# Optimization experiments

Measured on AMD Instinct MI355X. Metric: run time of the kernel, lower is better.

The kernel has to match this reference:

```python
import jax, jax.numpy as jnp
import numpy as np

NUM_EMBEDDINGS = 1024
EMBEDDING_DIM = 64
COMMITMENT_COST = 0.25
N_TOKENS = 131072


def setup_inputs() -> dict:
    key = jax.random.key(0)
    k_in, k_emb = jax.random.split(key)
    inputs = jax.random.normal(k_in, (N_TOKENS, EMBEDDING_DIM), dtype=jnp.float32)
    # torch init: uniform(-1/K, 1/K)
    codebook = jax.random.uniform(
        k_emb, (NUM_EMBEDDINGS, EMBEDDING_DIM), dtype=jnp.float32,
        minval=-1.0 / NUM_EMBEDDINGS, maxval=1.0 / NUM_EMBEDDINGS)
    return {"inputs": inputs, "codebook": codebook}


def reference(inputs, codebook):
    sg = jax.lax.stop_gradient
    distances = (jnp.sum(inputs * inputs, axis=1, keepdims=True)
                 - 2.0 * jnp.matmul(inputs, codebook.T)
                 + jnp.sum(codebook * codebook, axis=1)[None, :])
    encoding_indices = jnp.argmin(distances, axis=1)          # [N]
    # direct gather (same math as one-hot @ codebook)
    quantized = jnp.take(codebook, encoding_indices, axis=0)  # [N, D]
    # original computes e_latent_loss and q_latent_loss identically
    # (both mse(inputs, quantized.detach())), so loss = (1 + beta) * mse
    mse = jnp.mean((sg(quantized) - inputs) ** 2)
    loss = mse + COMMITMENT_COST * mse
    # straight-through estimator
    quantized_st = inputs + sg(quantized - inputs)
    # perplexity from code usage histogram (== mean of one-hot encodings)
    counts = jax.ops.segment_sum(
        jnp.ones((inputs.shape[0],), dtype=jnp.float32),
        encoding_indices, num_segments=NUM_EMBEDDINGS)
    avg_probs = counts / inputs.shape[0]
    perplexity = jnp.exp(-jnp.sum(avg_probs * jnp.log(avg_probs + 1e-10)))
    return loss, quantized_st, perplexity, encoding_indices[:, None]
```

## Files before the change

kernel.cpp:

```cpp
#include <hip/hip_runtime.h>
#include <math.h>

#define NTOK 131072
#define KC   1024
#define DIMV 64
#define NWAVE 8
#define TPW  64
#define TPB  512
#define CMAX 256
#define EPSH 1e-3f

#define OUT_LOSS 0
#define OUT_Q    1
#define OUT_PERP (1 + NTOK * DIMV)
#define OUT_IDX  (2 + NTOK * DIMV)

typedef __attribute__((ext_vector_type(8))) short short8;
typedef __attribute__((ext_vector_type(4))) float f32x4;

__device__ __forceinline__ float sumsq64_np(const float v[DIMV]) {
#pragma clang fp contract(off)
  {
    float r[8];
#pragma unroll
    for (int j = 0; j < 8; ++j) r[j] = v[j] * v[j];
#pragma unroll
    for (int i = 8; i < 64; i += 8) {
#pragma unroll
      for (int j = 0; j < 8; ++j) r[j] += v[i + j] * v[i + j];
    }
    return ((r[0] + r[1]) + (r[2] + r[3])) + ((r[4] + r[5]) + (r[6] + r[7]));
  }
}

__device__ __forceinline__ unsigned short bf16rne(float f) {
  unsigned int u = __float_as_uint(f);
  return (unsigned short)((u + 0x7fffu + ((u >> 16) & 1u)) >> 16);
}

__global__ void __launch_bounds__(512)
vq_fused(const float* __restrict__ xin, const float* __restrict__ cb,
         float* __restrict__ out, float* __restrict__ ws) {
  __shared__ __align__(16) char s_pack[131072];
  __shared__ float s_norm[KC];
  __shared__ unsigned int s_hist[KC];
  __shared__ unsigned int s_cand[NWAVE][CMAX];
  __shared__ unsigned long long s_key[NWAVE][TPW];
  __shared__ int s_cnt[NWAVE];
  __shared__ int s_last;

  const int tid = threadIdx.x;
  const int l   = tid & 63;
  const int wv  = tid >> 6;
  const int cls = l & 15;
  const int g   = l >> 4;
  const int blk = blockIdx.x;
  const int tb  = blk * TPB + wv * TPW;

  float* ws_mse = ws;
  unsigned int* ws_hist = (unsigned int*)ws + 1;
  unsigned int* ws_done = (unsigned int*)ws + 1 + KC;

  for (int c = tid; c < 8192; c += 512) {
    const int tile = c >> 7, f = (c >> 6) & 1, cl = c & 63;
    const int code = tile * 16 + (cl & 15);
    const int kb = f * 32 + (cl >> 4) * 8;
    const float4* src = (const float4*)(cb + code * DIMV + kb);
    float4 v0 = src[0], v1 = src[1];
    float v[8] = {v0.x, v0.y, v0.z, v0.w, v1.x, v1.y, v1.z, v1.w};
    unsigned int hw[4];
#pragma unroll
    for (int j = 0; j < 4; ++j) {
      hw[j] = (unsigned int)bf16rne(v[2 * j]) |
              ((unsigned int)bf16rne(v[2 * j + 1]) << 16);
    }
    *(uint4*)(s_pack + tile * 2048 + f * 1024 + cl * 16) =
        make_uint4(hw[0], hw[1], hw[2], hw[3]);
  }
  for (int k = tid; k < KC; k += 512) {
    float row[DIMV];
    const float4* r4 = (const float4*)(cb + (size_t)k * DIMV);
#pragma unroll
    for (int i = 0; i < 16; ++i) {
      float4 t = r4[i];
      row[4 * i + 0] = t.x; row[4 * i + 1] = t.y;
      row[4 * i + 2] = t.z; row[4 * i + 3] = t.w;
    }
    s_norm[k] = sumsq64_np(row);
    s_hist[k] = 0u;
  }
  s_key[wv][l] = ~0ull;
  if (tid < NWAVE) s_cnt[tid] = 0;

  short8 af[4][2];
#pragma unroll
  for (int grp = 0; grp < 4; ++grp) {
    const float* xr = xin + (size_t)(tb + grp * 16 + cls) * DIMV + g * 8;
#pragma unroll
    for (int kc = 0; kc < 2; ++kc) {
      float4 v0 = *(const float4*)(xr + kc * 32);
      float4 v1 = *(const float4*)(xr + kc * 32 + 4);
      float vv[8] = {v0.x, v0.y, v0.z, v0.w, v1.x, v1.y, v1.z, v1.w};
#pragma unroll
      for (int j = 0; j < 8; ++j) af[grp][kc][j] = (short)bf16rne(vv[j]);
    }
  }
  __syncthreads();

  float minv[4][4];
#pragma unroll
  for (int grp = 0; grp < 4; ++grp)
#pragma unroll
    for (int j = 0; j < 4; ++j) minv[grp][j] = INFINITY;

  short8 b0 = *(const short8*)(s_pack + l * 16);
  short8 b1 = *(const short8*)(s_pack + 1024 + l * 16);
  float nr = s_norm[cls];
#pragma unroll 2
  for (int t = 0; t < 63; ++t) {
    short8 c0 = b0, c1 = b1;
    float cc = -0.5f * nr;
    const char* bp = s_pack + (t + 1) * 2048 + l * 16;
    b0 = *(const short8*)(bp);
    b1 = *(const short8*)(bp + 1024);
    nr = s_norm[(t + 1) * 16 + cls];
#pragma unroll
    for (int grp = 0; grp < 4; ++grp) {
      f32x4 acc = {cc, cc, cc, cc};
      acc = __builtin_amdgcn_mfma_f32_16x16x32_bf16(af[grp][0], c0, acc, 0, 0, 0);
      acc = __builtin_amdgcn_mfma_f32_16x16x32_bf16(af[grp][1], c1, acc, 0, 0, 0);
#pragma unroll
      for (int j = 0; j < 4; ++j)
        minv[grp][j] = fminf(minv[grp][j], -acc[j]);
    }
  }
  {
    float cc = -0.5f * nr;
#pragma unroll
    for (int grp = 0; grp < 4; ++grp) {
      f32x4 acc = {cc, cc, cc, cc};
      acc = __builtin_amdgcn_mfma_f32_16x16x32_bf16(af[grp][0], b0, acc, 0, 0, 0);
      acc = __builtin_amdgcn_mfma_f32_16x16x32_bf16(af[grp][1], b1, acc, 0, 0, 0);
#pragma unroll
      for (int j = 0; j < 4; ++j)
        minv[grp][j] = fminf(minv[grp][j], -acc[j]);
    }
  }
#pragma unroll
  for (int mask = 1; mask < 16; mask <<= 1) {
#pragma unroll
    for (int grp = 0; grp < 4; ++grp)
#pragma unroll
      for (int j = 0; j < 4; ++j)
        minv[grp][j] = fminf(minv[grp][j], __shfl_xor(minv[grp][j], mask, 64));
  }
  float thr[4][4];
#pragma unroll
  for (int grp = 0; grp < 4; ++grp)
#pragma unroll
    for (int j = 0; j < 4; ++j) thr[grp][j] = minv[grp][j] + EPSH;

  b0 = *(const short8*)(s_pack + l * 16);
  b1 = *(const short8*)(s_pack + 1024 + l * 16);
  nr = s_norm[cls];
#pragma unroll 2
  for (int t = 0; t < 64; ++t) {
    short8 c0 = b0, c1 = b1;
    float cc = -0.5f * nr;
    if (t < 63) {
      const char* bp = s_pack + (t + 1) * 2048 + l * 16;
      b0 = *(const short8*)(bp);
      b1 = *(const short8*)(bp + 1024);
      nr = s_norm[(t + 1) * 16 + cls];
    }
#pragma unroll
    for (int grp = 0; grp < 4; ++grp) {
      f32x4 acc = {cc, cc, cc, cc};
      acc = __builtin_amdgcn_mfma_f32_16x16x32_bf16(af[grp][0], c0, acc, 0, 0, 0);
      acc = __builtin_amdgcn_mfma_f32_16x16x32_bf16(af[grp][1], c1, acc, 0, 0, 0);
#pragma unroll
      for (int j = 0; j < 4; ++j) {
        if (-acc[j] <= thr[grp][j]) {
          int pos = atomicAdd(&s_cnt[wv], 1);
          if (pos < CMAX)
            s_cand[wv][pos] =
                ((unsigned int)(grp * 16 + g * 4 + j) << 10) |
                (unsigned int)(t * 16 + cls);
        }
      }
    }
  }
  asm volatile("s_waitcnt lgkmcnt(0)" ::: "memory");
  const int cnt = s_cnt[wv];
  int n = cnt < CMAX ? cnt : CMAX;

  for (int base = 0; base < n; base += 64) {
    int i = base + l;
    if (i < n) {
      unsigned int pk = s_cand[wv][i];
      int m = (int)(pk >> 10), k = (int)(pk & 1023);
      const float4* xr4 = (const float4*)(xin + (size_t)(tb + m) * DIMV);
      const float4* er4 = (const float4*)(cb + (size_t)k * DIMV);
      float r[8];
      float dot = 0.0f;
#pragma unroll
      for (int s = 0; s < 8; ++s) {
        float4 a = xr4[2 * s], b = xr4[2 * s + 1];
        float4 ea = er4[2 * s], eb = er4[2 * s + 1];
        float xv[8] = {a.x, a.y, a.z, a.w, b.x, b.y, b.z, b.w};
        float ev[8] = {ea.x, ea.y, ea.z, ea.w, eb.x, eb.y, eb.z, eb.w};
        {
#pragma clang fp contract(off)
#pragma unroll
          for (int j = 0; j < 8; ++j) {
            float sq = xv[j] * xv[j];
            r[j] = (s == 0) ? sq : (r[j] + sq);
          }
        }
#pragma unroll
        for (int j = 0; j < 8; ++j) dot = __builtin_fmaf(ev[j], xv[j], dot);
      }
      float xx = ((r[0] + r[1]) + (r[2] + r[3])) + ((r[4] + r[5]) + (r[6] + r[7]));
      float d = (xx - 2.0f * dot) + s_norm[k];
      unsigned long long key =
          ((unsigned long long)__float_as_uint(d) << 10) | (unsigned long long)k;
      atomicMin(&s_key[wv][m], key);
    }
  }

  if (cnt > CMAX) {
    asm volatile("s_waitcnt lgkmcnt(0)" ::: "memory");
    const int m = l;
    float xv[DIMV];
    const float4* xr4 = (const float4*)(xin + (size_t)(tb + m) * DIMV);
#pragma unroll
    for (int i = 0; i < 16; ++i) {
      float4 t4 = xr4[i];
      xv[4 * i + 0] = t4.x; xv[4 * i + 1] = t4.y;
      xv[4 * i + 2] = t4.z; xv[4 * i + 3] = t4.w;
    }
    float xx = sumsq64_np(xv);
    float bd = INFINITY; int bk = 0;
    for (int k = 0; k < KC; ++k) {
      const float* e = cb + (size_t)k * DIMV;
      float dot = 0.0f;
#pragma unroll
      for (int i = 0; i < DIMV; ++i) dot = __builtin_fmaf(e[i], xv[i], dot);
      float d = (xx - 2.0f * dot) + s_norm[k];
      if (d < bd) { bd = d; bk = k; }
    }
    s_key[wv][m] =
        ((unsigned long long)__float_as_uint(bd) << 10) | (unsigned long long)bk;
  }
  asm volatile("s_waitcnt lgkmcnt(0)" ::: "memory");

  {
    const int token = tb + l;
    unsigned long long key = s_key[wv][l];
    const int bk = (int)(key & 1023ull);
    out[OUT_IDX + token] = (float)bk;
    atomicAdd(&s_hist[bk], 1u);
    const float4* q4 = (const float4*)(cb + (size_t)bk * DIMV);
    const float4* x4 = (const float4*)(xin + (size_t)token * DIMV);
    float* oq = out + OUT_Q + (size_t)token * DIMV;
    float mse_part = 0.0f;
#pragma unroll
    for (int rr = 0; rr < 16; ++rr) {
      float4 qv = q4[rr], xv = x4[rr];
      float d0 = qv.x - xv.x, d1 = qv.y - xv.y;
      float d2 = qv.z - xv.z, d3 = qv.w - xv.w;
      float4 o;
      o.x = xv.x + d0; o.y = xv.y + d1; o.z = xv.z + d2; o.w = xv.w + d3;
      mse_part = __builtin_fmaf(d0, d0, mse_part);
      mse_part = __builtin_fmaf(d1, d1, mse_part);
      mse_part = __builtin_fmaf(d2, d2, mse_part);
      mse_part = __builtin_fmaf(d3, d3, mse_part);
      *(float4*)(oq + 4 * rr) = o;
    }
#pragma unroll
    for (int mask = 1; mask < 64; mask <<= 1)
      mse_part += __shfl_xor(mse_part, mask, 64);
    if (l == 0) atomicAdd(ws_mse, mse_part);
  }

  __syncthreads();
  for (int k = tid; k < KC; k += 512) {
    unsigned int c = s_hist[k];
    if (c) atomicAdd(&ws_hist[k], c);
  }
  __syncthreads();

  if (tid == 0) {
    __threadfence();
    unsigned int tkt = atomicAdd(ws_done, 1u);
    s_last = (tkt == (unsigned int)(gridDim.x - 1)) ? 1 : 0;
  }
  __syncthreads();
  if (s_last) {
    __threadfence();
    float term = 0.0f;
    for (int k = tid; k < KC; k += 512) {
      unsigned int c = atomicAdd(&ws_hist[k], 0u);
      float p = (float)c / 131072.0f;
      term += p * logf(p + 1e-10f);
    }
    s_norm[tid] = term;
    __syncthreads();
#pragma unroll
    for (int s = 256; s > 0; s >>= 1) {
      if (tid < s) s_norm[tid] += s_norm[tid + s];
      __syncthreads();
    }
    if (tid == 0) {
      out[OUT_PERP] = expf(-s_norm[0]);
      float mse = atomicAdd(ws_mse, 0.0f) / 8388608.0f;
      out[OUT_LOSS] = mse + 0.25f * mse;
    }
  }
}

extern "C" void kernel_launch(void* const* d_in, const int* in_sizes, int n_in,
                              void* d_out, int out_size, void* d_ws, size_t ws_size,
                              hipStream_t stream) {
  (void)in_sizes; (void)n_in; (void)out_size; (void)ws_size;
  const float* xin = (const float*)d_in[0];
  const float* cb  = (const float*)d_in[1];
  float* out = (float*)d_out;
  float* ws  = (float*)d_ws;

  hipMemsetAsync(d_ws, 0, sizeof(float) * (1 + KC + 1), stream);
  hipLaunchKernelGGL(vq_fused, dim3(NTOK / TPB), dim3(512), 0, stream,
                     xin, cb, out, ws);
}
```

Baseline: 203.7 us.

## Split codebook scan across wave pairs with 1024-thread blocks

Doubles the block to 1024 threads so that each group of 64 tokens is handled by two waves, each scanning half of the codebook tiles. Per-wave minima are merged through shared memory before the candidate-threshold pass. The epilogue then has two threads per token writing halves of the output row. This aims to raise the number of waves per CU and cut per-wave MFMA latency, given that the 131 KB codebook in shared memory limits the CU to one block. The cost is extra block-wide syncs, a smaller candidate buffer per wave that makes the slow fallback path more likely, and higher register pressure under the 1024-thread launch bound.

```diff
diff --git a/kernel.cpp b/kernel.cpp
--- a/kernel.cpp
+++ b/kernel.cpp
@@ -4,10 +4,8 @@
 #define NTOK 131072
 #define KC   1024
 #define DIMV 64
-#define NWAVE 8
-#define TPW  64
 #define TPB  512
-#define CMAX 256
+#define CMAX 128
 #define EPSH 1e-3f
 
 #define OUT_LOSS 0
@@ -38,15 +36,17 @@
   return (unsigned short)((u + 0x7fffu + ((u >> 16) & 1u)) >> 16);
 }
 
-__global__ void __launch_bounds__(512)
+__global__ void __launch_bounds__(1024)
 vq_fused(const float* __restrict__ xin, const float* __restrict__ cb,
          float* __restrict__ out, float* __restrict__ ws) {
   __shared__ __align__(16) char s_pack[131072];
   __shared__ float s_norm[KC];
   __shared__ unsigned int s_hist[KC];
-  __shared__ unsigned int s_cand[NWAVE][CMAX];
-  __shared__ unsigned long long s_key[NWAVE][TPW];
-  __shared__ int s_cnt[NWAVE];
+  __shared__ float s_pmin[16][64];
+  __shared__ float s_gmin[8][64];
+  __shared__ unsigned int s_cand[16][CMAX];
+  __shared__ unsigned long long s_key[8][64];
+  __shared__ int s_cnt[16];
   __shared__ int s_last;
 
   const int tid = threadIdx.x;
@@ -54,14 +54,16 @@
   const int wv  = tid >> 6;
   const int cls = l & 15;
   const int g   = l >> 4;
+  const int q   = wv >> 1;
+  const int wl  = wv & 1;
   const int blk = blockIdx.x;
-  const int tb  = blk * TPB + wv * TPW;
+  const int tb  = blk * TPB + q * 64;
 
   float* ws_mse = ws;
   unsigned int* ws_hist = (unsigned int*)ws + 1;
   unsigned int* ws_done = (unsigned int*)ws + 1 + KC;
 
-  for (int c = tid; c < 8192; c += 512) {
+  for (int c = tid; c < 8192; c += 1024) {
     const int tile = c >> 7, f = (c >> 6) & 1, cl = c & 63;
     const int code = tile * 16 + (cl & 15);
     const int kb = f * 32 + (cl >> 4) * 8;
@@ -77,7 +79,8 @@
     *(uint4*)(s_pack + tile * 2048 + f * 1024 + cl * 16) =
         make_uint4(hw[0], hw[1], hw[2], hw[3]);
   }
-  for (int k = tid; k < KC; k += 512) {
+  {
+    const int k = tid;
     float row[DIMV];
     const float4* r4 = (const float4*)(cb + (size_t)k * DIMV);
 #pragma unroll
@@ -89,8 +92,8 @@
     s_norm[k] = sumsq64_np(row);
     s_hist[k] = 0u;
   }
-  s_key[wv][l] = ~0ull;
-  if (tid < NWAVE) s_cnt[tid] = 0;
+  if (tid < 512) s_key[tid >> 6][tid & 63] = ~0ull;
+  if (tid < 16) s_cnt[tid] = 0;
 
   short8 af[4][2];
 #pragma unroll
@@ -107,23 +110,26 @@
   }
   __syncthreads();
 
+  const int tbase = wl * 32;
   float minv[4][4];
 #pragma unroll
   for (int grp = 0; grp < 4; ++grp)
 #pragma unroll
     for (int j = 0; j < 4; ++j) minv[grp][j] = INFINITY;
 
-  short8 b0 = *(const short8*)(s_pack + l * 16);
-  short8 b1 = *(const short8*)(s_pack + 1024 + l * 16);
-  float nr = s_norm[cls];
+  short8 b0 = *(const short8*)(s_pack + tbase * 2048 + l * 16);
+  short8 b1 = *(const short8*)(s_pack + tbase * 2048 + 1024 + l * 16);
+  float nr = s_norm[tbase * 16 + cls];
 #pragma unroll 2
-  for (int t = 0; t < 63; ++t) {
+  for (int t = 0; t < 32; ++t) {
     short8 c0 = b0, c1 = b1;
     float cc = -0.5f * nr;
-    const char* bp = s_pack + (t + 1) * 2048 + l * 16;
-    b0 = *(const short8*)(bp);
-    b1 = *(const short8*)(bp + 1024);
-    nr = s_norm[(t + 1) * 16 + cls];
+    if (t < 31) {
+      const char* bp = s_pack + (tbase + t + 1) * 2048 + l * 16;
+      b0 = *(const short8*)(bp);
+      b1 = *(const short8*)(bp + 1024);
+      nr = s_norm[(tbase + t + 1) * 16 + cls];
+    }
 #pragma unroll
     for (int grp = 0; grp < 4; ++grp) {
       f32x4 acc = {cc, cc, cc, cc};
@@ -134,18 +140,6 @@
         minv[grp][j] = fminf(minv[grp][j], -acc[j]);
     }
   }
-  {
-    float cc = -0.5f * nr;
-#pragma unroll
-    for (int grp = 0; grp < 4; ++grp) {
-      f32x4 acc = {cc, cc, cc, cc};
-      acc = __builtin_amdgcn_mfma_f32_16x16x32_bf16(af[grp][0], b0, acc, 0, 0, 0);
-      acc = __builtin_amdgcn_mfma_f32_16x16x32_bf16(af[grp][1], b1, acc, 0, 0, 0);
-#pragma unroll
-      for (int j = 0; j < 4; ++j)
-        minv[grp][j] = fminf(minv[grp][j], -acc[j]);
-    }
-  }
 #pragma unroll
   for (int mask = 1; mask < 16; mask <<= 1) {
 #pragma unroll
@@ -154,24 +148,38 @@
       for (int j = 0; j < 4; ++j)
         minv[grp][j] = fminf(minv[grp][j], __shfl_xor(minv[grp][j], mask, 64));
   }
-  float thr[4][4];
-#pragma unroll
-  for (int grp = 0; grp < 4; ++grp)
-#pragma unroll
-    for (int j = 0; j < 4; ++j) thr[grp][j] = minv[grp][j] + EPSH;
-
-  b0 = *(const short8*)(s_pack + l * 16);
-  b1 = *(const short8*)(s_pack + 1024 + l * 16);
-  nr = s_norm[cls];
+  if (cls == 0) {
+#pragma unroll
+    for (int grp = 0; grp < 4; ++grp) {
+      float4 v = make_float4(minv[grp][0], minv[grp][1], minv[grp][2], minv[grp][3]);
+      *(float4*)&s_pmin[wv][grp * 16 + g * 4] = v;
+    }
+  }
+  __syncthreads();
+  if (tid < 512) {
+    const int q2 = tid >> 6, m = tid & 63;
+    s_gmin[q2][m] = fminf(s_pmin[q2 * 2][m], s_pmin[q2 * 2 + 1][m]);
+  }
+  __syncthreads();
+#pragma unroll
+  for (int grp = 0; grp < 4; ++grp) {
+    float4 t4 = *(const float4*)&s_gmin[q][grp * 16 + g * 4];
+    minv[grp][0] = t4.x + EPSH; minv[grp][1] = t4.y + EPSH;
+    minv[grp][2] = t4.z + EPSH; minv[grp][3] = t4.w + EPSH;
+  }
+
+  b0 = *(const short8*)(s_pack + tbase * 2048 + l * 16);
+  b1 = *(const short8*)(s_pack + tbase * 2048 + 1024 + l * 16);
+  nr = s_norm[tbase * 16 + cls];
 #pragma unroll 2
-  for (int t = 0; t < 64; ++t) {
+  for (int t = 0; t < 32; ++t) {
     short8 c0 = b0, c1 = b1;
     float cc = -0.5f * nr;
-    if (t < 63) {
-      const char* bp = s_pack + (t + 1) * 2048 + l * 16;
+    if (t < 31) {
+      const char* bp = s_pack + (tbase + t + 1) * 2048 + l * 16;
       b0 = *(const short8*)(bp);
       b1 = *(const short8*)(bp + 1024);
-      nr = s_norm[(t + 1) * 16 + cls];
+      nr = s_norm[(tbase + t + 1) * 16 + cls];
     }
 #pragma unroll
     for (int grp = 0; grp < 4; ++grp) {
@@ -180,12 +188,12 @@
       acc = __builtin_amdgcn_mfma_f32_16x16x32_bf16(af[grp][1], c1, acc, 0, 0, 0);
 #pragma unroll
       for (int j = 0; j < 4; ++j) {
-        if (-acc[j] <= thr[grp][j]) {
+        if (-acc[j] <= minv[grp][j]) {
           int pos = atomicAdd(&s_cnt[wv], 1);
           if (pos < CMAX)
             s_cand[wv][pos] =
                 ((unsigned int)(grp * 16 + g * 4 + j) << 10) |
-                (unsigned int)(t * 16 + cls);
+                (unsigned int)((tbase + t) * 16 + cls);
         }
       }
     }
@@ -224,12 +232,11 @@
       float d = (xx - 2.0f * dot) + s_norm[k];
       unsigned long long key =
           ((unsigned long long)__float_as_uint(d) << 10) | (unsigned long long)k;
-      atomicMin(&s_key[wv][m], key);
+      atomicMin(&s_key[q][m], key);
     }
   }
 
   if (cnt > CMAX) {
-    asm volatile("s_waitcnt lgkmcnt(0)" ::: "memory");
     const int m = l;
     float xv[DIMV];
     const float4* xr4 = (const float4*)(xin + (size_t)(tb + m) * DIMV);
@@ -241,7 +248,7 @@
     }
     float xx = sumsq64_np(xv);
     float bd = INFINITY; int bk = 0;
-    for (int k = 0; k < KC; ++k) {
+    for (int k = wl * 512; k < wl * 512 + 512; ++k) {
       const float* e = cb + (size_t)k * DIMV;
       float dot = 0.0f;
 #pragma unroll
@@ -249,23 +256,27 @@
       float d = (xx - 2.0f * dot) + s_norm[k];
       if (d < bd) { bd = d; bk = k; }
     }
-    s_key[wv][m] =
+    unsigned long long key =
         ((unsigned long long)__float_as_uint(bd) << 10) | (unsigned long long)bk;
-  }
-  asm volatile("s_waitcnt lgkmcnt(0)" ::: "memory");
+    atomicMin(&s_key[q][m], key);
+  }
+  __syncthreads();
 
   {
-    const int token = tb + l;
-    unsigned long long key = s_key[wv][l];
+    const int tok = tid >> 1, h = tid & 1;
+    const int token = blk * TPB + tok;
+    unsigned long long key = s_key[tok >> 6][tok & 63];
     const int bk = (int)(key & 1023ull);
-    out[OUT_IDX + token] = (float)bk;
-    atomicAdd(&s_hist[bk], 1u);
-    const float4* q4 = (const float4*)(cb + (size_t)bk * DIMV);
-    const float4* x4 = (const float4*)(xin + (size_t)token * DIMV);
-    float* oq = out + OUT_Q + (size_t)token * DIMV;
+    if (h == 0) {
+      out[OUT_IDX + token] = (float)bk;
+      atomicAdd(&s_hist[bk], 1u);
+    }
+    const float4* q4 = (const float4*)(cb + (size_t)bk * DIMV + h * 32);
+    const float4* x4 = (const float4*)(xin + (size_t)token * DIMV + h * 32);
+    float* oq = out + OUT_Q + (size_t)token * DIMV + h * 32;
     float mse_part = 0.0f;
 #pragma unroll
-    for (int rr = 0; rr < 16; ++rr) {
+    for (int rr = 0; rr < 8; ++rr) {
       float4 qv = q4[rr], xv = x4[rr];
       float d0 = qv.x - xv.x, d1 = qv.y - xv.y;
       float d2 = qv.z - xv.z, d3 = qv.w - xv.w;
@@ -282,13 +293,11 @@
       mse_part += __shfl_xor(mse_part, mask, 64);
     if (l == 0) atomicAdd(ws_mse, mse_part);
   }
-
-  __syncthreads();
-  for (int k = tid; k < KC; k += 512) {
-    unsigned int c = s_hist[k];
-    if (c) atomicAdd(&ws_hist[k], c);
-  }
-  __syncthreads();
+  __syncthreads();
+  {
+    unsigned int c = s_hist[tid];
+    if (c) atomicAdd(&ws_hist[tid], c);
+  }
 
   if (tid == 0) {
     __threadfence();
@@ -298,16 +307,12 @@
   __syncthreads();
   if (s_last) {
     __threadfence();
-    float term = 0.0f;
-    for (int k = tid; k < KC; k += 512) {
-      unsigned int c = atomicAdd(&ws_hist[k], 0u);
-      float p = (float)c / 131072.0f;
-      term += p * logf(p + 1e-10f);
-    }
-    s_norm[tid] = term;
+    unsigned int c = atomicAdd(&ws_hist[tid], 0u);
+    float p = (float)c / 131072.0f;
+    s_norm[tid] = p * logf(p + 1e-10f);
     __syncthreads();
 #pragma unroll
-    for (int s = 256; s > 0; s >>= 1) {
+    for (int s = 512; s > 0; s >>= 1) {
       if (tid < s) s_norm[tid] += s_norm[tid + s];
       __syncthreads();
     }
@@ -329,6 +334,6 @@
   float* ws  = (float*)d_ws;
 
   hipMemsetAsync(d_ws, 0, sizeof(float) * (1 + KC + 1), stream);
-  hipLaunchKernelGGL(vq_fused, dim3(NTOK / TPB), dim3(512), 0, stream,
+  hipLaunchKernelGGL(vq_fused, dim3(NTOK / TPB), dim3(1024), 0, stream,
                      xin, cb, out, ws);
 }
```

New measurement: 216.4 us. 6.2% more time.

## Precompute bf16 codebook pack in separate kernel and use 1024-thread blocks

Applied to the files above, without the earlier changes.

Moves the per-block bf16 codebook packing and norm computation into a small pre-kernel that writes to workspace, so each main block only copies the packed codebook into LDS. The main kernel switches to 16 waves of 32 tokens (1024 threads per block), which spreads the packing cost over more tokens and gives more waves per CU for the MFMA loops. It also replaces the memset with zeroing done in the pre-kernel. The trade-off is an extra launch, fewer independent MFMA groups per wave, and a smaller candidate buffer that may hit the slow fallback more often.

```diff
diff --git a/kernel.cpp b/kernel.cpp
--- a/kernel.cpp
+++ b/kernel.cpp
@@ -4,10 +4,10 @@
 #define NTOK 131072
 #define KC   1024
 #define DIMV 64
-#define NWAVE 8
-#define TPW  64
-#define TPB  512
-#define CMAX 256
+#define NWAVE 16
+#define TPW  32
+#define TPB  (NWAVE * TPW)
+#define CMAX 128
 #define EPSH 1e-3f
 
 #define OUT_LOSS 0
@@ -15,6 +15,11 @@
 #define OUT_PERP (1 + NTOK * DIMV)
 #define OUT_IDX  (2 + NTOK * DIMV)
 
+#define WS_HIST 1
+#define WS_TKT  1025
+#define WS_NORM 1026
+#define WS_PACK_BYTES 12288
+
 typedef __attribute__((ext_vector_type(8))) short short8;
 typedef __attribute__((ext_vector_type(4))) float f32x4;
 
@@ -38,9 +43,41 @@
   return (unsigned short)((u + 0x7fffu + ((u >> 16) & 1u)) >> 16);
 }
 
-__global__ void __launch_bounds__(512)
-vq_fused(const float* __restrict__ xin, const float* __restrict__ cb,
-         float* __restrict__ out, float* __restrict__ ws) {
+__global__ void __launch_bounds__(256)
+vq_pack_kernel(const float* __restrict__ cb, float* __restrict__ ws) {
+  const int e = blockIdx.x * 256 + threadIdx.x;
+  if (e < 1026) ws[e] = 0.0f;
+  const int tile = e >> 7, f = (e >> 6) & 1, l = e & 63;
+  const int code = tile * 16 + (l & 15);
+  const int kb = f * 32 + (l >> 4) * 8;
+  const float4* src = reinterpret_cast<const float4*>(cb + code * DIMV + kb);
+  float4 v0 = src[0], v1 = src[1];
+  float v[8] = {v0.x, v0.y, v0.z, v0.w, v1.x, v1.y, v1.z, v1.w};
+  unsigned int hw[4];
+#pragma unroll
+  for (int j = 0; j < 4; ++j) {
+    hw[j] = (unsigned int)bf16rne(v[2 * j]) |
+            ((unsigned int)bf16rne(v[2 * j + 1]) << 16);
+  }
+  char* pack = (char*)ws + WS_PACK_BYTES;
+  *(uint4*)(pack + tile * 2048 + f * 1024 + l * 16) =
+      make_uint4(hw[0], hw[1], hw[2], hw[3]);
+  if (e < KC) {
+    float row[DIMV];
+    const float4* r4 = reinterpret_cast<const float4*>(cb + e * DIMV);
+#pragma unroll
+    for (int i = 0; i < 16; ++i) {
+      float4 t = r4[i];
+      row[4 * i + 0] = t.x; row[4 * i + 1] = t.y;
+      row[4 * i + 2] = t.z; row[4 * i + 3] = t.w;
+    }
+    ws[WS_NORM + e] = sumsq64_np(row);
+  }
+}
+
+__global__ void __launch_bounds__(1024)
+vq_main_mfma(const float* __restrict__ xin, const float* __restrict__ cb,
+             float* __restrict__ out, float* __restrict__ ws) {
   __shared__ __align__(16) char s_pack[131072];
   __shared__ float s_norm[KC];
   __shared__ unsigned int s_hist[KC];
@@ -58,43 +95,26 @@
   const int tb  = blk * TPB + wv * TPW;
 
   float* ws_mse = ws;
-  unsigned int* ws_hist = (unsigned int*)ws + 1;
-  unsigned int* ws_done = (unsigned int*)ws + 1 + KC;
-
-  for (int c = tid; c < 8192; c += 512) {
-    const int tile = c >> 7, f = (c >> 6) & 1, cl = c & 63;
-    const int code = tile * 16 + (cl & 15);
-    const int kb = f * 32 + (cl >> 4) * 8;
-    const float4* src = (const float4*)(cb + code * DIMV + kb);
-    float4 v0 = src[0], v1 = src[1];
-    float v[8] = {v0.x, v0.y, v0.z, v0.w, v1.x, v1.y, v1.z, v1.w};
-    unsigned int hw[4];
-#pragma unroll
-    for (int j = 0; j < 4; ++j) {
-      hw[j] = (unsigned int)bf16rne(v[2 * j]) |
-              ((unsigned int)bf16rne(v[2 * j + 1]) << 16);
-    }
-    *(uint4*)(s_pack + tile * 2048 + f * 1024 + cl * 16) =
-        make_uint4(hw[0], hw[1], hw[2], hw[3]);
-  }
-  for (int k = tid; k < KC; k += 512) {
-    float row[DIMV];
-    const float4* r4 = (const float4*)(cb + (size_t)k * DIMV);
-#pragma unroll
-    for (int i = 0; i < 16; ++i) {
-      float4 t = r4[i];
-      row[4 * i + 0] = t.x; row[4 * i + 1] = t.y;
-      row[4 * i + 2] = t.z; row[4 * i + 3] = t.w;
-    }
-    s_norm[k] = sumsq64_np(row);
-    s_hist[k] = 0u;
-  }
-  s_key[wv][l] = ~0ull;
+  unsigned int* ws_hist = (unsigned int*)ws + WS_HIST;
+  unsigned int* ws_done = (unsigned int*)ws + WS_TKT;
+  const float* ws_norm = ws + WS_NORM;
+  const char* pack = (const char*)ws + WS_PACK_BYTES;
+
+  {
+    const uint4* src = (const uint4*)pack;
+    uint4* dst = (uint4*)s_pack;
+#pragma unroll
+    for (int i = 0; i < 8; ++i) dst[tid + i * 1024] = src[tid + i * 1024];
+  }
+  s_norm[tid] = ws_norm[tid];
+  s_hist[tid] = 0u;
+  if (tid < NWAVE * TPW) s_key[tid >> 5][tid & 31] = ~0ull;
   if (tid < NWAVE) s_cnt[tid] = 0;
-
-  short8 af[4][2];
-#pragma unroll
-  for (int grp = 0; grp < 4; ++grp) {
+  __syncthreads();
+
+  short8 af[2][2];
+#pragma unroll
+  for (int grp = 0; grp < 2; ++grp) {
     const float* xr = xin + (size_t)(tb + grp * 16 + cls) * DIMV + g * 8;
 #pragma unroll
     for (int kc = 0; kc < 2; ++kc) {
@@ -105,11 +125,10 @@
       for (int j = 0; j < 8; ++j) af[grp][kc][j] = (short)bf16rne(vv[j]);
     }
   }
-  __syncthreads();
-
-  float minv[4][4];
-#pragma unroll
-  for (int grp = 0; grp < 4; ++grp)
+
+  float minv[2][4];
+#pragma unroll
+  for (int grp = 0; grp < 2; ++grp)
 #pragma unroll
     for (int j = 0; j < 4; ++j) minv[grp][j] = INFINITY;
 
@@ -117,15 +136,17 @@
   short8 b1 = *(const short8*)(s_pack + 1024 + l * 16);
   float nr = s_norm[cls];
 #pragma unroll 2
-  for (int t = 0; t < 63; ++t) {
+  for (int t = 0; t < 64; ++t) {
     short8 c0 = b0, c1 = b1;
     float cc = -0.5f * nr;
-    const char* bp = s_pack + (t + 1) * 2048 + l * 16;
-    b0 = *(const short8*)(bp);
-    b1 = *(const short8*)(bp + 1024);
-    nr = s_norm[(t + 1) * 16 + cls];
-#pragma unroll
-    for (int grp = 0; grp < 4; ++grp) {
+    if (t < 63) {
+      const char* bp = s_pack + (t + 1) * 2048 + l * 16;
+      b0 = *(const short8*)(bp);
+      b1 = *(const short8*)(bp + 1024);
+      nr = s_norm[(t + 1) * 16 + cls];
+    }
+#pragma unroll
+    for (int grp = 0; grp < 2; ++grp) {
       f32x4 acc = {cc, cc, cc, cc};
       acc = __builtin_amdgcn_mfma_f32_16x16x32_bf16(af[grp][0], c0, acc, 0, 0, 0);
       acc = __builtin_amdgcn_mfma_f32_16x16x32_bf16(af[grp][1], c1, acc, 0, 0, 0);
@@ -134,29 +155,17 @@
         minv[grp][j] = fminf(minv[grp][j], -acc[j]);
     }
   }
-  {
-    float cc = -0.5f * nr;
-#pragma unroll
-    for (int grp = 0; grp < 4; ++grp) {
-      f32x4 acc = {cc, cc, cc, cc};
-      acc = __builtin_amdgcn_mfma_f32_16x16x32_bf16(af[grp][0], b0, acc, 0, 0, 0);
-      acc = __builtin_amdgcn_mfma_f32_16x16x32_bf16(af[grp][1], b1, acc, 0, 0, 0);
-#pragma unroll
-      for (int j = 0; j < 4; ++j)
-        minv[grp][j] = fminf(minv[grp][j], -acc[j]);
-    }
-  }
 #pragma unroll
   for (int mask = 1; mask < 16; mask <<= 1) {
 #pragma unroll
-    for (int grp = 0; grp < 4; ++grp)
+    for (int grp = 0; grp < 2; ++grp)
 #pragma unroll
       for (int j = 0; j < 4; ++j)
         minv[grp][j] = fminf(minv[grp][j], __shfl_xor(minv[grp][j], mask, 64));
   }
-  float thr[4][4];
-#pragma unroll
-  for (int grp = 0; grp < 4; ++grp)
+  float thr[2][4];
+#pragma unroll
+  for (int grp = 0; grp < 2; ++grp)
 #pragma unroll
     for (int j = 0; j < 4; ++j) thr[grp][j] = minv[grp][j] + EPSH;
 
@@ -174,7 +183,7 @@
       nr = s_norm[(t + 1) * 16 + cls];
     }
 #pragma unroll
-    for (int grp = 0; grp < 4; ++grp) {
+    for (int grp = 0; grp < 2; ++grp) {
       f32x4 acc = {cc, cc, cc, cc};
       acc = __builtin_amdgcn_mfma_f32_16x16x32_bf16(af[grp][0], c0, acc, 0, 0, 0);
       acc = __builtin_amdgcn_mfma_f32_16x16x32_bf16(af[grp][1], c1, acc, 0, 0, 0);
@@ -230,42 +239,47 @@
 
   if (cnt > CMAX) {
     asm volatile("s_waitcnt lgkmcnt(0)" ::: "memory");
-    const int m = l;
-    float xv[DIMV];
-    const float4* xr4 = (const float4*)(xin + (size_t)(tb + m) * DIMV);
-#pragma unroll
-    for (int i = 0; i < 16; ++i) {
-      float4 t4 = xr4[i];
-      xv[4 * i + 0] = t4.x; xv[4 * i + 1] = t4.y;
-      xv[4 * i + 2] = t4.z; xv[4 * i + 3] = t4.w;
-    }
-    float xx = sumsq64_np(xv);
-    float bd = INFINITY; int bk = 0;
-    for (int k = 0; k < KC; ++k) {
-      const float* e = cb + (size_t)k * DIMV;
-      float dot = 0.0f;
-#pragma unroll
-      for (int i = 0; i < DIMV; ++i) dot = __builtin_fmaf(e[i], xv[i], dot);
-      float d = (xx - 2.0f * dot) + s_norm[k];
-      if (d < bd) { bd = d; bk = k; }
-    }
-    s_key[wv][m] =
-        ((unsigned long long)__float_as_uint(bd) << 10) | (unsigned long long)bk;
+    if (l < TPW) {
+      const int m = l;
+      float xv[DIMV];
+      const float4* xr4 = (const float4*)(xin + (size_t)(tb + m) * DIMV);
+#pragma unroll
+      for (int i = 0; i < 16; ++i) {
+        float4 t4 = xr4[i];
+        xv[4 * i + 0] = t4.x; xv[4 * i + 1] = t4.y;
+        xv[4 * i + 2] = t4.z; xv[4 * i + 3] = t4.w;
+      }
+      float xx = sumsq64_np(xv);
+      float bd = INFINITY; int bk = 0;
+      for (int k = 0; k < KC; ++k) {
+        const float* e = cb + (size_t)k * DIMV;
+        float dot = 0.0f;
+#pragma unroll
+        for (int i = 0; i < DIMV; ++i) dot = __builtin_fmaf(e[i], xv[i], dot);
+        float d = (xx - 2.0f * dot) + s_norm[k];
+        if (d < bd) { bd = d; bk = k; }
+      }
+      s_key[wv][m] =
+          ((unsigned long long)__float_as_uint(bd) << 10) | (unsigned long long)bk;
+    }
   }
   asm volatile("s_waitcnt lgkmcnt(0)" ::: "memory");
 
   {
-    const int token = tb + l;
-    unsigned long long key = s_key[wv][l];
+    const int m = l & 31, h = l >> 5;
+    const int token = tb + m;
+    unsigned long long key = s_key[wv][m];
     const int bk = (int)(key & 1023ull);
-    out[OUT_IDX + token] = (float)bk;
-    atomicAdd(&s_hist[bk], 1u);
-    const float4* q4 = (const float4*)(cb + (size_t)bk * DIMV);
-    const float4* x4 = (const float4*)(xin + (size_t)token * DIMV);
-    float* oq = out + OUT_Q + (size_t)token * DIMV;
+    if (h == 0) {
+      out[OUT_IDX + token] = (float)bk;
+      atomicAdd(&s_hist[bk], 1u);
+    }
+    const float4* q4 = (const float4*)(cb + (size_t)bk * DIMV + h * 32);
+    const float4* x4 = (const float4*)(xin + (size_t)token * DIMV + h * 32);
+    float* oq = out + OUT_Q + (size_t)token * DIMV + h * 32;
     float mse_part = 0.0f;
 #pragma unroll
-    for (int rr = 0; rr < 16; ++rr) {
+    for (int rr = 0; rr < 8; ++rr) {
       float4 qv = q4[rr], xv = x4[rr];
       float d0 = qv.x - xv.x, d1 = qv.y - xv.y;
       float d2 = qv.z - xv.z, d3 = qv.w - xv.w;
@@ -284,11 +298,10 @@
   }
 
   __syncthreads();
-  for (int k = tid; k < KC; k += 512) {
-    unsigned int c = s_hist[k];
-    if (c) atomicAdd(&ws_hist[k], c);
-  }
-  __syncthreads();
+  {
+    unsigned int c = s_hist[tid];
+    if (c) atomicAdd(&ws_hist[tid], c);
+  }
 
   if (tid == 0) {
     __threadfence();
@@ -298,16 +311,12 @@
   __syncthreads();
   if (s_last) {
     __threadfence();
-    float term = 0.0f;
-    for (int k = tid; k < KC; k += 512) {
-      unsigned int c = atomicAdd(&ws_hist[k], 0u);
-      float p = (float)c / 131072.0f;
-      term += p * logf(p + 1e-10f);
-    }
-    s_norm[tid] = term;
+    unsigned int c = atomicAdd(&ws_hist[tid], 0u);
+    float p = (float)c / 131072.0f;
+    s_norm[tid] = p * logf(p + 1e-10f);
     __syncthreads();
 #pragma unroll
-    for (int s = 256; s > 0; s >>= 1) {
+    for (int s = 512; s > 0; s >>= 1) {
       if (tid < s) s_norm[tid] += s_norm[tid + s];
       __syncthreads();
     }
@@ -328,7 +337,7 @@
   float* out = (float*)d_out;
   float* ws  = (float*)d_ws;
 
-  hipMemsetAsync(d_ws, 0, sizeof(float) * (1 + KC + 1), stream);
-  hipLaunchKernelGGL(vq_fused, dim3(NTOK / TPB), dim3(512), 0, stream,
+  hipLaunchKernelGGL(vq_pack_kernel, dim3(32), dim3(256), 0, stream, cb, ws);
+  hipLaunchKernelGGL(vq_main_mfma, dim3(NTOK / TPB), dim3(1024), 0, stream,
                      xin, cb, out, ws);
 }
```

Result: faster. 181.2 us (-11.0%).
